# Performance work log

Measured on AMD Instinct MI355X. Metric: run time of the kernel, lower is better.

Reference implementation:

```python
import math
import jax, jax.numpy as jnp
import numpy as np

N_LAYER = 4
D = 256            # n_embd
NH = 4             # n_head
MLP_MULT = 128
VOCAB = 256
N = D * MLP_MULT // NH   # 8192 neurons per head
LN_EPS = 1e-5
TWO_PI = 2.0 * math.pi


def get_freqs(n, theta=2.0 ** 16):
    # quantize(arange(n), q=2) = floor(t/2)*2
    t = jnp.floor(jnp.arange(n, dtype=jnp.float32) / 2.0) * 2.0
    return 1.0 / theta ** (t / n) / TWO_PI


def layernorm(x):
    # nn.LayerNorm(D, elementwise_affine=False): plain normalization
    m = jnp.mean(x, axis=-1, keepdims=True)
    v = jnp.var(x, axis=-1, keepdims=True)
    return (x - m) / jnp.sqrt(v + LN_EPS)


def rope(phases, v):
    # v_rot interleaves (-v_odd, v_even) pairs
    v_rot = jnp.stack((-v[..., 1::2], v[..., ::2]), axis=-1).reshape(v.shape)
    p = (phases % 1.0) * TWO_PI
    return v * jnp.cos(p) + v_rot * jnp.sin(p)


def attention(x_sparse, x):
    # Q = K = x_sparse: (B, nh, T, N); V = x: (B, 1, T, D)
    T = x_sparse.shape[2]
    freqs = get_freqs(N).reshape(1, 1, 1, N)
    phases = jnp.arange(T, dtype=jnp.float32).reshape(1, 1, T, 1) * freqs
    QR = rope(phases, x_sparse)                       # (B, nh, T, N)
    scores = jnp.einsum('bhtn,bhsn->bhts', QR, QR)    # (B, nh, T, T)
    mask = jnp.tril(jnp.ones((T, T), dtype=bool), k=-1)  # strict lower tri
    scores = jnp.where(mask, scores, 0.0)
    return scores @ x                                 # (B, nh, T, D), V broadcast over heads


def bdh_forward(idx, embed, encoder, encoder_v, decoder, lm_head):
    B, T = idx.shape
    x = embed[idx][:, None]        # (B, 1, T, D)
    x = layernorm(x)
    dec = decoder.reshape(NH, N, D)
    for _ in range(N_LAYER):
        x_latent = jnp.einsum('btd,hdn->bhtn', x[:, 0], encoder)   # D -> N expand
        x_sparse = jax.nn.relu(x_latent)
        yKV = attention(x_sparse, x)                               # (B, nh, T, D)
        yKV = layernorm(yKV)
        y_latent = jnp.einsum('bhtd,hdn->bhtn', yKV, encoder_v)
        y_sparse = jax.nn.relu(y_latent)
        xy_sparse = x_sparse * y_sparse                            # gate
        yMLP = jnp.einsum('bhtn,hnd->btd', xy_sparse, dec)         # N -> D decode
        x = layernorm(x + yMLP[:, None])                           # residual + LN
    logits = x[:, 0] @ lm_head    # (B, T, vocab)
    return logits


def setup_inputs() -> dict:
    key = jax.random.key(0)
    k1, k2, k3, k4, k5, k6 = jax.random.split(key, 6)
    B, T = 2, 512
    std = 0.02
    return {
        'idx': jax.random.randint(k1, (B, T), 0, VOCAB, dtype=jnp.int64 if jax.config.jax_enable_x64 else jnp.int32),
        'embed': jax.random.normal(k2, (VOCAB, D), dtype=jnp.float32) * std,
        'encoder': jax.random.normal(k3, (NH, D, N), dtype=jnp.float32) * std,
        'encoder_v': jax.random.normal(k4, (NH, D, N), dtype=jnp.float32) * std,
        'decoder': jax.random.normal(k5, (NH * N, D), dtype=jnp.float32) * std,
        'lm_head': jax.random.normal(k6, (D, VOCAB), dtype=jnp.float32) * std,
    }


def reference(idx, embed, encoder, encoder_v, decoder, lm_head):
    return bdh_forward(idx, embed, encoder, encoder_v, decoder, lm_head)
```

## Files before the change

kernel.cpp:

```cpp
#include <hip/hip_runtime.h>
#include <hip/hip_bf16.h>
#include <cstdio>

#define DEV static __device__ __forceinline__

typedef __attribute__((ext_vector_type(4))) float floatx4;
typedef __attribute__((ext_vector_type(8))) __bf16 bf16x8;

constexpr int Bv = 2, Tv = 512, Dv = 256, NHv = 4, Nv = 8192, NLv = 4, Vv = 256;
constexpr int BTv = Bv * Tv;
constexpr int BHv = Bv * NHv;
constexpr float LNEPS = 1e-5f;
constexpr int KS_SC = 8;
constexpr int KS_DEC = 8;

DEV float b2f(short s) {
    unsigned u = ((unsigned)(unsigned short)s) << 16;
    return __builtin_bit_cast(float, u);
}
DEV short f2b(float f) {
    unsigned u = __builtin_bit_cast(unsigned, f);
    u = (u + 0x7fffu + ((u >> 16) & 1u)) >> 16;
    return (short)u;
}

__global__ __launch_bounds__(256) void k_cvtT(const float* __restrict__ in,
                                              short* __restrict__ out, int R, int C) {
    __shared__ float tile[32][33];
    const float* ib = in + (size_t)blockIdx.z * R * C;
    short* ob = out + (size_t)blockIdx.z * R * C;
    int c0 = blockIdx.x * 32, r0 = blockIdx.y * 32;
    int tx = threadIdx.x & 31, ty = threadIdx.x >> 5;
#pragma unroll
    for (int i = 0; i < 4; i++) {
        int r = r0 + ty + i * 8;
        tile[ty + i * 8][tx] = ib[(size_t)r * C + c0 + tx];
    }
    __syncthreads();
#pragma unroll
    for (int i = 0; i < 4; i++) {
        int c = c0 + ty + i * 8;
        ob[(size_t)c * R + r0 + tx] = f2b(tile[tx][ty + i * 8]);
    }
}

__global__ __launch_bounds__(256) void k_transp(const short* __restrict__ xb,
                                                short* __restrict__ xbT) {
    __shared__ short tile[32][33];
    int b = blockIdx.z;
    int t0 = blockIdx.x * 32, d0 = blockIdx.y * 32;
    int tx = threadIdx.x & 31, ty = threadIdx.x >> 5;
#pragma unroll
    for (int i = 0; i < 4; i++)
        tile[ty + i * 8][tx] = xb[((size_t)b * Tv + t0 + ty + i * 8) * Dv + d0 + tx];
    __syncthreads();
#pragma unroll
    for (int i = 0; i < 4; i++)
        xbT[((size_t)b * Dv + d0 + ty + i * 8) * Tv + t0 + tx] = tile[tx][ty + i * 8];
}

__global__ __launch_bounds__(256) void k_rope(float2* __restrict__ tab) {
    int i = blockIdx.x * 256 + threadIdx.x;
    int t = blockIdx.y;
    float f = exp2f(-(float)i / 256.0f) * 0.15915494309189535f;
    float ph = fmodf((float)t * f, 1.0f) * 6.2831853071795864f;
    tab[(size_t)t * (Nv / 2) + i] = make_float2(cosf(ph), sinf(ph));
}

DEV void reduce2(float& s1, float& s2) {
    __shared__ float r1[4];
    __shared__ float r2[4];
#pragma unroll
    for (int o = 32; o > 0; o >>= 1) {
        s1 += __shfl_down(s1, o, 64);
        s2 += __shfl_down(s2, o, 64);
    }
    int lane = threadIdx.x & 63, w = threadIdx.x >> 6;
    if (lane == 0) { r1[w] = s1; r2[w] = s2; }
    __syncthreads();
    s1 = r1[0] + r1[1] + r1[2] + r1[3];
    s2 = r2[0] + r2[1] + r2[2] + r2[3];
}

DEV float ln_val(float v, float s1, float s2) {
    float m = s1 * (1.0f / Dv);
    float var = s2 * (1.0f / Dv) - m * m;
    float inv = rsqrtf(var + LNEPS);
    return (v - m) * inv;
}

__global__ __launch_bounds__(256) void k_embed_ln(const int* __restrict__ idx,
                                                  const float* __restrict__ embed,
                                                  float* __restrict__ xf, short* __restrict__ xb) {
    int r = blockIdx.x, d = threadIdx.x;
    float v = embed[(size_t)idx[r] * Dv + d];
    float s1 = v, s2 = v * v;
    reduce2(s1, s2);
    float o = ln_val(v, s1, s2);
    xf[(size_t)r * Dv + d] = o;
    xb[(size_t)r * Dv + d] = f2b(o);
}

__global__ __launch_bounds__(256) void k_ln(const float* __restrict__ in,
                                            short* __restrict__ outb) {
    int r = blockIdx.x, d = threadIdx.x;
    size_t o = (size_t)r * Dv + d;
    float v = in[o];
    float s1 = v, s2 = v * v;
    reduce2(s1, s2);
    outb[o] = f2b(ln_val(v, s1, s2));
}

__global__ __launch_bounds__(256) void k_lnsum(const short* __restrict__ ymb,
                                               float* __restrict__ xf, short* __restrict__ xb) {
    int r = blockIdx.x, d = threadIdx.x;
    size_t o = (size_t)r * Dv + d;
    float v = xf[o];
#pragma unroll
    for (int z = 0; z < NHv * KS_DEC; z++)
        v += b2f(ymb[(size_t)z * BTv * Dv + o]);
    float s1 = v, s2 = v * v;
    reduce2(s1, s2);
    float res = ln_val(v, s1, s2);
    xf[o] = res;
    xb[o] = f2b(res);
}

DEV void gemm_main(const short* __restrict__ Ab, int lda,
                   const short* __restrict__ Bb, int ldb, int K,
                   short* sA, short* sB, floatx4 acc[4][4]) {
    const int tid = threadIdx.x;
    const int lane = tid & 63, w = tid >> 6;
    const int wr = w >> 1, wc = w & 1;
    const int lrow = lane & 15, koff = (lane >> 4) * 8;
    for (int kk = 0; kk < K; kk += 32) {
        __syncthreads();
#pragma unroll
        for (int p = 0; p < 2; p++) {
            int c = tid + p * 256;
            int row = c >> 2, kc = c & 3;
            *(int4*)&sA[row * 40 + kc * 8] = *(const int4*)&Ab[(size_t)row * lda + kk + kc * 8];
            *(int4*)&sB[row * 40 + kc * 8] = *(const int4*)&Bb[(size_t)row * ldb + kk + kc * 8];
        }
        __syncthreads();
        bf16x8 aF[4], bF[4];
#pragma unroll
        for (int m = 0; m < 4; m++) aF[m] = *(const bf16x8*)&sA[(wr * 64 + m * 16 + lrow) * 40 + koff];
#pragma unroll
        for (int n = 0; n < 4; n++) bF[n] = *(const bf16x8*)&sB[(wc * 64 + n * 16 + lrow) * 40 + koff];
#pragma unroll
        for (int m = 0; m < 4; m++)
#pragma unroll
            for (int n = 0; n < 4; n++)
                acc[m][n] = __builtin_amdgcn_mfma_f32_16x16x32_bf16(aF[m], bF[n], acc[m][n], 0, 0, 0);
    }
}

__global__ __launch_bounds__(256) void k_latent(const short* __restrict__ xb,
                                                const short* __restrict__ encT,
                                                const float2* __restrict__ ropeT,
                                                short* __restrict__ xs,
                                                short* __restrict__ qr) {
    __shared__ short sA[128 * 40];
    __shared__ short sB[128 * 40];
    int bid = blockIdx.x;
    int xcd = bid & 7, rr = bid >> 3;
    int cmb = xcd + 8 * (rr & 31);
    int mb = rr >> 5;
    int nb = cmb & 63, h = cmb >> 6;
    const short* Ab = xb + (size_t)mb * 128 * Dv;
    const short* Bb = encT + (size_t)h * Nv * Dv + (size_t)nb * 128 * Dv;
    floatx4 acc[4][4] = {};
    gemm_main(Ab, Dv, Bb, Dv, Dv, sA, sB, acc);
    int lane = threadIdx.x & 63, w = threadIdx.x >> 6, wr = w >> 1, wc = w & 1;
    int rb = (lane >> 4) * 4, cb = lane & 15;
    float sgn = (cb & 1) ? 1.0f : -1.0f;
#pragma unroll
    for (int m = 0; m < 4; m++)
#pragma unroll
        for (int n = 0; n < 4; n++)
#pragma unroll
            for (int r = 0; r < 4; r++) {
                int row = mb * 128 + wr * 64 + m * 16 + rb + r;
                int col = nb * 128 + wc * 64 + n * 16 + cb;
                int b = row >> 9, t = row & 511;
                float v = acc[m][n][r];
                v = v > 0.f ? v : 0.f;
                float vp = __shfl_xor(v, 1);
                float2 cs = ropeT[(size_t)t * (Nv / 2) + (col >> 1)];
                float o = v * cs.x + sgn * vp * cs.y;
                size_t idx = ((size_t)(b * NHv + h) * Tv + t) * Nv + col;
                xs[idx] = f2b(v);
                qr[idx] = f2b(o);
            }
}

__global__ __launch_bounds__(256) void k_scores(const short* __restrict__ qr,
                                                short* __restrict__ scs) {
    __shared__ short sA[128 * 40];
    __shared__ short sB[128 * 40];
    int bid = blockIdx.x;
    int xcd = bid & 7, rr = bid >> 3;
    int cmb = xcd + 8 * (rr & 7);
    int pb = rr >> 3;
    int bh = cmb & 7, ks = cmb >> 3;
    int tb = 0;
    while (((tb + 1) * (tb + 2)) / 2 <= pb) tb++;
    int sb = pb - (tb * (tb + 1)) / 2;
    const bool diag = (tb == sb);
    const int KC = Nv / KS_SC;
    const short* Ab = qr + ((size_t)bh * Tv + tb * 128) * Nv + ks * KC;
    const short* Bb = qr + ((size_t)bh * Tv + sb * 128) * Nv + ks * KC;
    floatx4 acc[4][4] = {};
    const int tid = threadIdx.x, lane = tid & 63, w = tid >> 6;
    const int wr = w >> 1, wc = w & 1;
    const int lrow = lane & 15, koff = (lane >> 4) * 8;
    for (int kk = 0; kk < KC; kk += 32) {
        __syncthreads();
#pragma unroll
        for (int p = 0; p < 2; p++) {
            int c = tid + p * 256;
            int row = c >> 2, kc = c & 3;
            *(int4*)&sA[row * 40 + kc * 8] = *(const int4*)&Ab[(size_t)row * Nv + kk + kc * 8];
            if (!diag)
                *(int4*)&sB[row * 40 + kc * 8] = *(const int4*)&Bb[(size_t)row * Nv + kk + kc * 8];
        }
        __syncthreads();
        const short* sBr = diag ? sA : sB;
        bf16x8 aF[4], bF[4];
#pragma unroll
        for (int m = 0; m < 4; m++) aF[m] = *(const bf16x8*)&sA[(wr * 64 + m * 16 + lrow) * 40 + koff];
#pragma unroll
        for (int n = 0; n < 4; n++) bF[n] = *(const bf16x8*)&sBr[(wc * 64 + n * 16 + lrow) * 40 + koff];
#pragma unroll
        for (int m = 0; m < 4; m++)
#pragma unroll
            for (int n = 0; n < 4; n++)
                acc[m][n] = __builtin_amdgcn_mfma_f32_16x16x32_bf16(aF[m], bF[n], acc[m][n], 0, 0, 0);
    }
    short* slab = scs + ((size_t)ks * BHv + bh) * Tv * Tv;
    int rb = (lane >> 4) * 4, cb = lane & 15;
#pragma unroll
    for (int m = 0; m < 4; m++)
#pragma unroll
        for (int n = 0; n < 4; n++)
#pragma unroll
            for (int r = 0; r < 4; r++) {
                int t = tb * 128 + wr * 64 + m * 16 + rb + r;
                int s = sb * 128 + wc * 64 + n * 16 + cb;
                slab[(size_t)t * Tv + s] = f2b(acc[m][n][r]);
            }
}

__global__ __launch_bounds__(256) void k_redsc(const short* __restrict__ scs,
                                               short* __restrict__ scb) {
    int c = blockIdx.x * 256 + threadIdx.x;
    int row = c >> 6;
    int s0 = (c & 63) * 8;
    int t = row & (Tv - 1);
    float a[8] = {};
#pragma unroll
    for (int ks = 0; ks < KS_SC; ks++) {
        int4 raw = *(const int4*)&scs[((size_t)ks * BHv * Tv + row) * Tv + s0];
        const short* rs = (const short*)&raw;
#pragma unroll
        for (int j = 0; j < 8; j++) a[j] += b2f(rs[j]);
    }
    union { short s[8]; int4 v; } u;
#pragma unroll
    for (int j = 0; j < 8; j++) u.s[j] = (s0 + j < t) ? f2b(a[j]) : 0;
    *(int4*)&scb[(size_t)row * Tv + s0] = u.v;
}

__global__ __launch_bounds__(256) void k_pvg(const short* __restrict__ scb,
                                             const short* __restrict__ xbT,
                                             float* __restrict__ ykv) {
    __shared__ short sA[128 * 40];
    __shared__ short sB[128 * 40];
    int mb = blockIdx.x, nb = blockIdx.y, bh = blockIdx.z;
    int b = bh >> 2;
    const short* Ab = scb + ((size_t)bh * Tv + mb * 128) * Tv;
    const short* Bb = xbT + ((size_t)b * Dv + nb * 128) * Tv;
    floatx4 acc[4][4] = {};
    gemm_main(Ab, Tv, Bb, Tv, Tv, sA, sB, acc);
    int lane = threadIdx.x & 63, w = threadIdx.x >> 6, wr = w >> 1, wc = w & 1;
    int rb = (lane >> 4) * 4, cb = lane & 15;
#pragma unroll
    for (int m = 0; m < 4; m++)
#pragma unroll
        for (int n = 0; n < 4; n++)
#pragma unroll
            for (int r = 0; r < 4; r++) {
                int t = mb * 128 + wr * 64 + m * 16 + rb + r;
                int d = nb * 128 + wc * 64 + n * 16 + cb;
                ykv[((size_t)bh * Tv + t) * Dv + d] = acc[m][n][r];
            }
}

__global__ __launch_bounds__(256) void k_gate(const short* __restrict__ ykvb,
                                              const short* __restrict__ encvT,
                                              short* __restrict__ xs) {
    __shared__ short sA[128 * 40];
    __shared__ short sB[128 * 40];
    int bid = blockIdx.x;
    int xcd = bid & 7, rr = bid >> 3;
    int cmb = xcd + 8 * (rr & 31);
    int wi = rr >> 5;
    int mb = wi & 3, bq = wi >> 2;
    int nb = cmb & 63, h = cmb >> 6;
    int bh = bq * NHv + h;
    const short* Ab = ykvb + ((size_t)bh * Tv + mb * 128) * Dv;
    const short* Bb = encvT + (size_t)h * Nv * Dv + (size_t)nb * 128 * Dv;
    floatx4 acc[4][4] = {};
    gemm_main(Ab, Dv, Bb, Dv, Dv, sA, sB, acc);
    int lane = threadIdx.x & 63, w = threadIdx.x >> 6, wr = w >> 1, wc = w & 1;
    int rb = (lane >> 4) * 4, cb = lane & 15;
#pragma unroll
    for (int m = 0; m < 4; m++)
#pragma unroll
        for (int n = 0; n < 4; n++)
#pragma unroll
            for (int r = 0; r < 4; r++) {
                int t = mb * 128 + wr * 64 + m * 16 + rb + r;
                int col = nb * 128 + wc * 64 + n * 16 + cb;
                size_t idx = ((size_t)bh * Tv + t) * Nv + col;
                float v = acc[m][n][r];
                v = v > 0.f ? v : 0.f;
                xs[idx] = f2b(v * b2f(xs[idx]));
            }
}

__global__ __launch_bounds__(256) void k_decode(const short* __restrict__ xy,
                                                const short* __restrict__ decT,
                                                short* __restrict__ ymb) {
    __shared__ short sA[128 * 40];
    __shared__ short sB[128 * 40];
    int bid = blockIdx.x;
    int xcd = bid & 7, rr = bid >> 3;
    int cmb = xcd + 8 * (rr & 7);
    int mb = rr >> 3;
    int nb = cmb & 1, h = (cmb >> 1) & 3, ks = cmb >> 3;
    const int KC = Nv / KS_DEC;
    int row0 = mb * 128;
    int b = row0 >> 9, t0 = row0 & 511;
    const short* Ab = xy + ((size_t)(b * NHv + h) * Tv + t0) * Nv + ks * KC;
    const short* Bb = decT + (size_t)h * Dv * Nv + (size_t)nb * 128 * Nv + ks * KC;
    floatx4 acc[4][4] = {};
    gemm_main(Ab, Nv, Bb, Nv, KC, sA, sB, acc);
    short* slab = ymb + (size_t)(h * KS_DEC + ks) * BTv * Dv;
    int lane = threadIdx.x & 63, w = threadIdx.x >> 6, wr = w >> 1, wc = w & 1;
    int rb = (lane >> 4) * 4, cb = lane & 15;
#pragma unroll
    for (int m = 0; m < 4; m++)
#pragma unroll
        for (int n = 0; n < 4; n++)
#pragma unroll
            for (int r = 0; r < 4; r++) {
                int row = row0 + wr * 64 + m * 16 + rb + r;
                int col = nb * 128 + wc * 64 + n * 16 + cb;
                slab[(size_t)row * Dv + col] = f2b(acc[m][n][r]);
            }
}

__global__ __launch_bounds__(256) void k_head(const short* __restrict__ xb,
                                              const short* __restrict__ lmhT,
                                              float* __restrict__ out) {
    __shared__ short sA[128 * 40];
    __shared__ short sB[128 * 40];
    int mb = blockIdx.x, nb = blockIdx.y;
    const short* Ab = xb + (size_t)mb * 128 * Dv;
    const short* Bb = lmhT + (size_t)nb * 128 * Dv;
    floatx4 acc[4][4] = {};
    gemm_main(Ab, Dv, Bb, Dv, Dv, sA, sB, acc);
    int lane = threadIdx.x & 63, w = threadIdx.x >> 6, wr = w >> 1, wc = w & 1;
    int rb = (lane >> 4) * 4, cb = lane & 15;
#pragma unroll
    for (int m = 0; m < 4; m++)
#pragma unroll
        for (int n = 0; n < 4; n++)
#pragma unroll
            for (int r = 0; r < 4; r++) {
                int row = mb * 128 + wr * 64 + m * 16 + rb + r;
                int col = nb * 128 + wc * 64 + n * 16 + cb;
                out[(size_t)row * Vv + col] = acc[m][n][r];
            }
}

extern "C" void kernel_launch(void* const* d_in, const int* in_sizes, int n_in,
                              void* d_out, int out_size, void* d_ws, size_t ws_size,
                              hipStream_t stream) {
    const int* idx = (const int*)d_in[0];
    const float* embed = (const float*)d_in[1];
    const float* enc = (const float*)d_in[2];
    const float* encv = (const float*)d_in[3];
    const float* dec = (const float*)d_in[4];
    const float* lmh = (const float*)d_in[5];
    float* out = (float*)d_out;

    char* w = (char*)d_ws;
    size_t off = 0;
    auto alloc = [&](size_t bytes) -> void* {
        void* p = w + off;
        off = (off + bytes + 255) & ~(size_t)255;
        return p;
    };
    short* encT = (short*)alloc((size_t)NHv * Nv * Dv * 2);
    short* encvT = (short*)alloc((size_t)NHv * Nv * Dv * 2);
    short* decT = (short*)alloc((size_t)NHv * Dv * Nv * 2);
    short* lmhT = (short*)alloc((size_t)Vv * Dv * 2);
    float2* ropeT = (float2*)alloc((size_t)Tv * (Nv / 2) * sizeof(float2));
    float* xf = (float*)alloc((size_t)BTv * Dv * 4);
    short* xb = (short*)alloc((size_t)BTv * Dv * 2);
    short* xbT = (short*)alloc((size_t)BTv * Dv * 2);
    short* xs = (short*)alloc((size_t)BHv * Tv * Nv * 2);
    short* qr = (short*)alloc((size_t)BHv * Tv * Nv * 2);
    short* scs = (short*)alloc((size_t)KS_SC * BHv * Tv * Tv * 2);
    short* scb = (short*)alloc((size_t)BHv * Tv * Tv * 2);
    float* ykvf = (float*)alloc((size_t)BHv * Tv * Dv * 4);
    short* ykvb = (short*)alloc((size_t)BHv * Tv * Dv * 2);
    short* ymb = (short*)alloc((size_t)NHv * KS_DEC * BTv * Dv * 2);
    if (off > ws_size) {
        fprintf(stderr, "BDH: workspace too small: need %zu, have %zu\n", off, ws_size);
        return;
    }

    k_cvtT<<<dim3(Nv / 32, Dv / 32, NHv), 256, 0, stream>>>(enc, encT, Dv, Nv);
    k_cvtT<<<dim3(Nv / 32, Dv / 32, NHv), 256, 0, stream>>>(encv, encvT, Dv, Nv);
    k_cvtT<<<dim3(Dv / 32, Nv / 32, NHv), 256, 0, stream>>>(dec, decT, Nv, Dv);
    k_cvtT<<<dim3(Vv / 32, Dv / 32, 1), 256, 0, stream>>>(lmh, lmhT, Dv, Vv);
    k_rope<<<dim3(Nv / 2 / 256, Tv), 256, 0, stream>>>(ropeT);
    k_embed_ln<<<BTv, 256, 0, stream>>>(idx, embed, xf, xb);

    for (int L = 0; L < NLv; L++) {
        k_latent<<<2048, 256, 0, stream>>>(xb, encT, ropeT, xs, qr);
        k_transp<<<dim3(Tv / 32, Dv / 32, Bv), 256, 0, stream>>>(xb, xbT);
        k_scores<<<640, 256, 0, stream>>>(qr, scs);
        k_redsc<<<(BHv * Tv * Tv / 8) / 256, 256, 0, stream>>>(scs, scb);
        k_pvg<<<dim3(Tv / 128, Dv / 128, BHv), 256, 0, stream>>>(scb, xbT, ykvf);
        k_ln<<<BHv * Tv, 256, 0, stream>>>(ykvf, ykvb);
        k_gate<<<2048, 256, 0, stream>>>(ykvb, encvT, xs);
        k_decode<<<512, 256, 0, stream>>>(xs, decT, ymb);
        k_lnsum<<<BTv, 256, 0, stream>>>(ymb, xf, xb);
    }
    k_head<<<dim3(BTv / 128, Vv / 128), 256, 0, stream>>>(xb, lmhT, out);
}
```

Baseline: 871.4 us.

## Stage GEMM epilogues through LDS for coalesced stores, recompute x_sparse from rotated Q

```diff
diff --git a/kernel.cpp b/kernel.cpp
--- a/kernel.cpp
+++ b/kernel.cpp
@@ -23,6 +23,7 @@
     u = (u + 0x7fffu + ((u >> 16) & 1u)) >> 16;
     return (short)u;
 }
+DEV int scol8(int c4) { return c4 < 8 ? c4 * 8 : 80 + (c4 - 8) * 8; }
 
 __global__ __launch_bounds__(256) void k_cvtT(const float* __restrict__ in,
                                               short* __restrict__ out, int R, int C) {
@@ -59,12 +60,14 @@
         xbT[((size_t)b * Dv + d0 + ty + i * 8) * Tv + t0 + tx] = tile[tx][ty + i * 8];
 }
 
-__global__ __launch_bounds__(256) void k_rope(float2* __restrict__ tab) {
+__global__ __launch_bounds__(256) void k_rope(unsigned* __restrict__ tab) {
     int i = blockIdx.x * 256 + threadIdx.x;
     int t = blockIdx.y;
     float f = exp2f(-(float)i / 256.0f) * 0.15915494309189535f;
     float ph = fmodf((float)t * f, 1.0f) * 6.2831853071795864f;
-    tab[(size_t)t * (Nv / 2) + i] = make_float2(cosf(ph), sinf(ph));
+    unsigned c = (unsigned short)f2b(cosf(ph));
+    unsigned s = (unsigned short)f2b(sinf(ph));
+    tab[(size_t)t * (Nv / 2) + i] = c | (s << 16);
 }
 
 DEV void reduce2(float& s1, float& s2) {
@@ -158,11 +161,11 @@
 
 __global__ __launch_bounds__(256) void k_latent(const short* __restrict__ xb,
                                                 const short* __restrict__ encT,
-                                                const float2* __restrict__ ropeT,
-                                                short* __restrict__ xs,
+                                                const unsigned* __restrict__ ropeT,
                                                 short* __restrict__ qr) {
     __shared__ short sA[128 * 40];
     __shared__ short sB[128 * 40];
+    __shared__ short sC[64][152];
     int bid = blockIdx.x;
     int xcd = bid & 7, rr = bid >> 3;
     int cmb = xcd + 8 * (rr & 31);
@@ -172,33 +175,48 @@
     const short* Bb = encT + (size_t)h * Nv * Dv + (size_t)nb * 128 * Dv;
     floatx4 acc[4][4] = {};
     gemm_main(Ab, Dv, Bb, Dv, Dv, sA, sB, acc);
-    int lane = threadIdx.x & 63, w = threadIdx.x >> 6, wr = w >> 1, wc = w & 1;
+    const int tid = threadIdx.x, lane = tid & 63, w = tid >> 6;
+    int wr = w >> 1, wc = w & 1;
     int rb = (lane >> 4) * 4, cb = lane & 15;
     float sgn = (cb & 1) ? 1.0f : -1.0f;
-#pragma unroll
-    for (int m = 0; m < 4; m++)
-#pragma unroll
-        for (int n = 0; n < 4; n++)
-#pragma unroll
-            for (int r = 0; r < 4; r++) {
-                int row = mb * 128 + wr * 64 + m * 16 + rb + r;
-                int col = nb * 128 + wc * 64 + n * 16 + cb;
-                int b = row >> 9, t = row & 511;
-                float v = acc[m][n][r];
-                v = v > 0.f ? v : 0.f;
-                float vp = __shfl_xor(v, 1);
-                float2 cs = ropeT[(size_t)t * (Nv / 2) + (col >> 1)];
-                float o = v * cs.x + sgn * vp * cs.y;
-                size_t idx = ((size_t)(b * NHv + h) * Tv + t) * Nv + col;
-                xs[idx] = f2b(v);
-                qr[idx] = f2b(o);
-            }
+    int b = mb >> 2, t0 = (mb & 3) * 128;
+    short* dst = qr + ((size_t)(b * NHv + h) * Tv + t0) * Nv + nb * 128;
+#pragma unroll
+    for (int half = 0; half < 2; half++) {
+        if (wr == half) {
+#pragma unroll
+            for (int m = 0; m < 4; m++)
+#pragma unroll
+                for (int n = 0; n < 4; n++) {
+                    int col = nb * 128 + wc * 64 + n * 16 + cb;
+#pragma unroll
+                    for (int r = 0; r < 4; r++) {
+                        int t = t0 + half * 64 + m * 16 + rb + r;
+                        float v = acc[m][n][r];
+                        v = v > 0.f ? v : 0.f;
+                        float vp = __shfl_xor(v, 1);
+                        unsigned cs = ropeT[(size_t)t * (Nv / 2) + (col >> 1)];
+                        float c = b2f((short)(cs & 0xffff)), s = b2f((short)(cs >> 16));
+                        sC[m * 16 + rb + r][wc * 80 + n * 16 + cb] = f2b(v * c + sgn * vp * s);
+                    }
+                }
+        }
+        __syncthreads();
+#pragma unroll
+        for (int q = 0; q < 4; q++) {
+            int item = q * 256 + tid;
+            int row = item >> 4, c4 = item & 15;
+            *(int4*)&dst[(size_t)(half * 64 + row) * Nv + c4 * 8] = *(const int4*)&sC[row][scol8(c4)];
+        }
+        __syncthreads();
+    }
 }
 
 __global__ __launch_bounds__(256) void k_scores(const short* __restrict__ qr,
                                                 short* __restrict__ scs) {
     __shared__ short sA[128 * 40];
     __shared__ short sB[128 * 40];
+    __shared__ short sC[64][152];
     int bid = blockIdx.x;
     int xcd = bid & 7, rr = bid >> 3;
     int cmb = xcd + 8 * (rr & 7);
@@ -238,18 +256,28 @@
             for (int n = 0; n < 4; n++)
                 acc[m][n] = __builtin_amdgcn_mfma_f32_16x16x32_bf16(aF[m], bF[n], acc[m][n], 0, 0, 0);
     }
-    short* slab = scs + ((size_t)ks * BHv + bh) * Tv * Tv;
     int rb = (lane >> 4) * 4, cb = lane & 15;
-#pragma unroll
-    for (int m = 0; m < 4; m++)
-#pragma unroll
-        for (int n = 0; n < 4; n++)
-#pragma unroll
-            for (int r = 0; r < 4; r++) {
-                int t = tb * 128 + wr * 64 + m * 16 + rb + r;
-                int s = sb * 128 + wc * 64 + n * 16 + cb;
-                slab[(size_t)t * Tv + s] = f2b(acc[m][n][r]);
-            }
+    short* dst = scs + ((size_t)ks * BHv + bh) * Tv * Tv + (size_t)tb * 128 * Tv + sb * 128;
+#pragma unroll
+    for (int half = 0; half < 2; half++) {
+        if (wr == half) {
+#pragma unroll
+            for (int m = 0; m < 4; m++)
+#pragma unroll
+                for (int n = 0; n < 4; n++)
+#pragma unroll
+                    for (int r = 0; r < 4; r++)
+                        sC[m * 16 + rb + r][wc * 80 + n * 16 + cb] = f2b(acc[m][n][r]);
+        }
+        __syncthreads();
+#pragma unroll
+        for (int q = 0; q < 4; q++) {
+            int item = q * 256 + tid;
+            int row = item >> 4, c4 = item & 15;
+            *(int4*)&dst[(size_t)(half * 64 + row) * Tv + c4 * 8] = *(const int4*)&sC[row][scol8(c4)];
+        }
+        __syncthreads();
+    }
 }
 
 __global__ __launch_bounds__(256) void k_redsc(const short* __restrict__ scs,
@@ -299,9 +327,12 @@
 
 __global__ __launch_bounds__(256) void k_gate(const short* __restrict__ ykvb,
                                               const short* __restrict__ encvT,
-                                              short* __restrict__ xs) {
+                                              const short* __restrict__ qr,
+                                              const unsigned* __restrict__ ropeT,
+                                              short* __restrict__ xy) {
     __shared__ short sA[128 * 40];
     __shared__ short sB[128 * 40];
+    __shared__ short sC[64][152];
     int bid = blockIdx.x;
     int xcd = bid & 7, rr = bid >> 3;
     int cmb = xcd + 8 * (rr & 31);
@@ -313,21 +344,51 @@
     const short* Bb = encvT + (size_t)h * Nv * Dv + (size_t)nb * 128 * Dv;
     floatx4 acc[4][4] = {};
     gemm_main(Ab, Dv, Bb, Dv, Dv, sA, sB, acc);
-    int lane = threadIdx.x & 63, w = threadIdx.x >> 6, wr = w >> 1, wc = w & 1;
+    const int tid = threadIdx.x, lane = tid & 63, w = tid >> 6;
+    int wr = w >> 1, wc = w & 1;
     int rb = (lane >> 4) * 4, cb = lane & 15;
-#pragma unroll
-    for (int m = 0; m < 4; m++)
-#pragma unroll
-        for (int n = 0; n < 4; n++)
-#pragma unroll
-            for (int r = 0; r < 4; r++) {
-                int t = mb * 128 + wr * 64 + m * 16 + rb + r;
-                int col = nb * 128 + wc * 64 + n * 16 + cb;
-                size_t idx = ((size_t)bh * Tv + t) * Nv + col;
-                float v = acc[m][n][r];
-                v = v > 0.f ? v : 0.f;
-                xs[idx] = f2b(v * b2f(xs[idx]));
-            }
+    float sgn = (cb & 1) ? 1.0f : -1.0f;
+    const short* qsrc = qr + ((size_t)bh * Tv + mb * 128) * Nv + nb * 128;
+    short* dst = xy + ((size_t)bh * Tv + mb * 128) * Nv + nb * 128;
+#pragma unroll
+    for (int half = 0; half < 2; half++) {
+#pragma unroll
+        for (int q = 0; q < 4; q++) {
+            int item = q * 256 + tid;
+            int row = item >> 4, c4 = item & 15;
+            *(int4*)&sC[row][scol8(c4)] = *(const int4*)&qsrc[(size_t)(half * 64 + row) * Nv + c4 * 8];
+        }
+        __syncthreads();
+        if (wr == half) {
+#pragma unroll
+            for (int m = 0; m < 4; m++)
+#pragma unroll
+                for (int n = 0; n < 4; n++) {
+                    int col = nb * 128 + wc * 64 + n * 16 + cb;
+#pragma unroll
+                    for (int r = 0; r < 4; r++) {
+                        int lr = m * 16 + rb + r;
+                        int t = mb * 128 + half * 64 + lr;
+                        float qv = b2f(sC[lr][wc * 80 + n * 16 + cb]);
+                        float qp = b2f(sC[lr][wc * 80 + n * 16 + (cb ^ 1)]);
+                        unsigned cs = ropeT[(size_t)t * (Nv / 2) + (col >> 1)];
+                        float c = b2f((short)(cs & 0xffff)), s = b2f((short)(cs >> 16));
+                        float xsr = qv * c - sgn * qp * s;
+                        float v = acc[m][n][r];
+                        v = v > 0.f ? v : 0.f;
+                        sC[lr][wc * 80 + n * 16 + cb] = f2b(v * xsr);
+                    }
+                }
+        }
+        __syncthreads();
+#pragma unroll
+        for (int q = 0; q < 4; q++) {
+            int item = q * 256 + tid;
+            int row = item >> 4, c4 = item & 15;
+            *(int4*)&dst[(size_t)(half * 64 + row) * Nv + c4 * 8] = *(const int4*)&sC[row][scol8(c4)];
+        }
+        __syncthreads();
+    }
 }
 
 __global__ __launch_bounds__(256) void k_decode(const short* __restrict__ xy,
@@ -335,6 +396,7 @@
                                                 short* __restrict__ ymb) {
     __shared__ short sA[128 * 40];
     __shared__ short sB[128 * 40];
+    __shared__ short sC[64][152];
     int bid = blockIdx.x;
     int xcd = bid & 7, rr = bid >> 3;
     int cmb = xcd + 8 * (rr & 7);
@@ -347,19 +409,30 @@
     const short* Bb = decT + (size_t)h * Dv * Nv + (size_t)nb * 128 * Nv + ks * KC;
     floatx4 acc[4][4] = {};
     gemm_main(Ab, Nv, Bb, Nv, KC, sA, sB, acc);
-    short* slab = ymb + (size_t)(h * KS_DEC + ks) * BTv * Dv;
-    int lane = threadIdx.x & 63, w = threadIdx.x >> 6, wr = w >> 1, wc = w & 1;
+    const int tid = threadIdx.x, lane = tid & 63, w = tid >> 6;
+    int wr = w >> 1, wc = w & 1;
     int rb = (lane >> 4) * 4, cb = lane & 15;
-#pragma unroll
-    for (int m = 0; m < 4; m++)
-#pragma unroll
-        for (int n = 0; n < 4; n++)
-#pragma unroll
-            for (int r = 0; r < 4; r++) {
-                int row = row0 + wr * 64 + m * 16 + rb + r;
-                int col = nb * 128 + wc * 64 + n * 16 + cb;
-                slab[(size_t)row * Dv + col] = f2b(acc[m][n][r]);
-            }
+    short* dst = ymb + (size_t)(h * KS_DEC + ks) * BTv * Dv + (size_t)row0 * Dv + nb * 128;
+#pragma unroll
+    for (int half = 0; half < 2; half++) {
+        if (wr == half) {
+#pragma unroll
+            for (int m = 0; m < 4; m++)
+#pragma unroll
+                for (int n = 0; n < 4; n++)
+#pragma unroll
+                    for (int r = 0; r < 4; r++)
+                        sC[m * 16 + rb + r][wc * 80 + n * 16 + cb] = f2b(acc[m][n][r]);
+        }
+        __syncthreads();
+#pragma unroll
+        for (int q = 0; q < 4; q++) {
+            int item = q * 256 + tid;
+            int row = item >> 4, c4 = item & 15;
+            *(int4*)&dst[(size_t)(half * 64 + row) * Dv + c4 * 8] = *(const int4*)&sC[row][scol8(c4)];
+        }
+        __syncthreads();
+    }
 }
 
 __global__ __launch_bounds__(256) void k_head(const short* __restrict__ xb,
@@ -408,11 +481,11 @@
     short* encvT = (short*)alloc((size_t)NHv * Nv * Dv * 2);
     short* decT = (short*)alloc((size_t)NHv * Dv * Nv * 2);
     short* lmhT = (short*)alloc((size_t)Vv * Dv * 2);
-    float2* ropeT = (float2*)alloc((size_t)Tv * (Nv / 2) * sizeof(float2));
+    unsigned* ropeT = (unsigned*)alloc((size_t)Tv * (Nv / 2) * 4);
     float* xf = (float*)alloc((size_t)BTv * Dv * 4);
     short* xb = (short*)alloc((size_t)BTv * Dv * 2);
     short* xbT = (short*)alloc((size_t)BTv * Dv * 2);
-    short* xs = (short*)alloc((size_t)BHv * Tv * Nv * 2);
+    short* xy = (short*)alloc((size_t)BHv * Tv * Nv * 2);
     short* qr = (short*)alloc((size_t)BHv * Tv * Nv * 2);
     short* scs = (short*)alloc((size_t)KS_SC * BHv * Tv * Tv * 2);
     short* scb = (short*)alloc((size_t)BHv * Tv * Tv * 2);
@@ -432,14 +505,14 @@
     k_embed_ln<<<BTv, 256, 0, stream>>>(idx, embed, xf, xb);
 
     for (int L = 0; L < NLv; L++) {
-        k_latent<<<2048, 256, 0, stream>>>(xb, encT, ropeT, xs, qr);
+        k_latent<<<2048, 256, 0, stream>>>(xb, encT, ropeT, qr);
         k_transp<<<dim3(Tv / 32, Dv / 32, Bv), 256, 0, stream>>>(xb, xbT);
         k_scores<<<640, 256, 0, stream>>>(qr, scs);
         k_redsc<<<(BHv * Tv * Tv / 8) / 256, 256, 0, stream>>>(scs, scb);
         k_pvg<<<dim3(Tv / 128, Dv / 128, BHv), 256, 0, stream>>>(scb, xbT, ykvf);
         k_ln<<<BHv * Tv, 256, 0, stream>>>(ykvf, ykvb);
-        k_gate<<<2048, 256, 0, stream>>>(ykvb, encvT, xs);
-        k_decode<<<512, 256, 0, stream>>>(xs, decT, ymb);
+        k_gate<<<2048, 256, 0, stream>>>(ykvb, encvT, qr, ropeT, xy);
+        k_decode<<<512, 256, 0, stream>>>(xy, decT, ymb);
         k_lnsum<<<BTv, 256, 0, stream>>>(ymb, xf, xb);
     }
     k_head<<<dim3(BTv / 128, Vv / 128), 256, 0, stream>>>(xb, lmhT, out);
```

Result: slower. 1.020 ms (+17.1%).
